# Optimization experiments

Hardware: AMD Instinct MI355X
Metric: run time of the kernel (lower is better)

The kernel has to match this reference:

```python
import jax, jax.numpy as jnp
import numpy as np

N_EMBD = 1024
N_HEAD = 16
HEAD_DIM = N_EMBD // N_HEAD


def setup_inputs() -> dict:
    key = jax.random.key(0)
    ks = jax.random.split(key, 5)
    B, T, C = 2, 2048, N_EMBD
    scale = 0.02
    return {
        "x": jax.random.normal(ks[0], (B, T, C), dtype=jnp.float32),
        "w_attn": jax.random.normal(ks[1], (C, 3 * C), dtype=jnp.float32) * scale,
        "b_attn": jax.random.normal(ks[2], (3 * C,), dtype=jnp.float32) * scale,
        "w_proj": jax.random.normal(ks[3], (C, C), dtype=jnp.float32) * scale,
        "b_proj": jax.random.normal(ks[4], (C,), dtype=jnp.float32) * scale,
    }


def reference(x, w_attn, b_attn, w_proj, b_proj):
    B, T, C = x.shape
    H, D = N_HEAD, HEAD_DIM
    qkv = x @ w_attn + b_attn  # [B,T,3C]
    q, k, v = jnp.split(qkv, 3, axis=-1)
    # [B,T,C] -> [B,H,T,D]
    q = q.reshape(B, T, H, D).transpose(0, 2, 1, 3)
    k = k.reshape(B, T, H, D).transpose(0, 2, 1, 3)
    v = v.reshape(B, T, H, D).transpose(0, 2, 1, 3)
    scores = jnp.einsum("bhqd,bhkd->bhqk", q, k) / jnp.sqrt(jnp.float32(D))
    causal = jnp.tril(jnp.ones((T, T), dtype=bool))
    scores = jnp.where(causal, scores, jnp.finfo(scores.dtype).min)
    attn = jax.nn.softmax(scores, axis=-1)
    y = jnp.einsum("bhqk,bhkd->bhqd", attn, v)  # [B,H,T,D]
    y = y.transpose(0, 2, 1, 3).reshape(B, T, C)
    return y @ w_proj + b_proj
```

## Files before the change

### kernel.cpp

```cpp
#include <hip/hip_runtime.h>

typedef unsigned short u16;
typedef u16 u16x4 __attribute__((ext_vector_type(4)));
typedef u16 u16x8 __attribute__((ext_vector_type(8)));
typedef __bf16 bf16x8 __attribute__((ext_vector_type(8)));
typedef float floatx4 __attribute__((ext_vector_type(4)));

#define N_EMBD 1024
#define N_HEAD 16
#define HEAD_DIM 64
#define SEQ 2048
#define BATCH 2
#define M_ROWS (BATCH * SEQ)

typedef __attribute__((address_space(1))) const unsigned char ga_t;
typedef __attribute__((address_space(3))) unsigned char la_t;

#if __has_builtin(__builtin_amdgcn_exp2f)
#define EXP2(x) __builtin_amdgcn_exp2f(x)
#else
#define EXP2(x) exp2f(x)
#endif

__device__ __forceinline__ float bf2f(u16 b) {
  return __uint_as_float(((unsigned)b) << 16);
}
__device__ __forceinline__ u16 f2bf(float f) {
  unsigned u = __float_as_uint(f);
  u += 0x7fffu + ((u >> 16) & 1u);
  return (u16)(u >> 16);
}

__global__ __launch_bounds__(256) void convert_x(const float* __restrict__ x,
                                                 u16* __restrict__ xb) {
  const long i = ((long)blockIdx.x * 256 + threadIdx.x) * 8;
  const float4 f0 = *(const float4*)&x[i];
  const float4 f1 = *(const float4*)&x[i + 4];
  u16x8 p;
  p[0] = f2bf(f0.x); p[1] = f2bf(f0.y); p[2] = f2bf(f0.z); p[3] = f2bf(f0.w);
  p[4] = f2bf(f1.x); p[5] = f2bf(f1.y); p[6] = f2bf(f1.z); p[7] = f2bf(f1.w);
  *(u16x8*)&xb[i] = p;
}

__global__ __launch_bounds__(256) void transpose2(
    const float* __restrict__ wa, const float* __restrict__ wp,
    u16* __restrict__ outa, u16* __restrict__ outp) {
  __shared__ u16 tile[32][33];
  const int R = N_EMBD;
  const float* in;
  u16* out;
  int C, bx;
  if (blockIdx.x < 96) {
    in = wa; out = outa; C = 3 * N_EMBD; bx = blockIdx.x * 32;
  } else {
    in = wp; out = outp; C = N_EMBD; bx = (blockIdx.x - 96) * 32;
  }
  const int by = blockIdx.y * 32;
  const int tx = threadIdx.x;
  const int ty = threadIdx.y;
#pragma unroll
  for (int j = 0; j < 32; j += 8)
    tile[ty + j][tx] = f2bf(in[(long)(by + ty + j) * C + bx + tx]);
  __syncthreads();
#pragma unroll
  for (int j = 0; j < 32; j += 8)
    out[(long)(bx + ty + j) * R + by + tx] = tile[tx][ty + j];
}

#define BK 32

template <int MODE>
__global__ __launch_bounds__(256) void gemm128(
    const u16* __restrict__ A, const u16* __restrict__ Bt,
    const float* __restrict__ bias, float* __restrict__ out,
    u16* __restrict__ qo, u16* __restrict__ ko, u16* __restrict__ vo, int N,
    int K) {
  __shared__ u16 As[128 * BK];
  __shared__ u16 Bs[128 * BK];
  const int tid = threadIdx.x;
  const int bm = blockIdx.y * 128;
  const int bn = blockIdx.x * 128;
  const int w = tid >> 6;
  const int l = tid & 63;
  const int wm = (w >> 1) * 64;
  const int wn = (w & 1) * 64;
  const int m16 = l & 15;
  const int quad = l >> 4;
  const int lrow = l >> 2;
  const int lcol = (l & 3) * 8;

  floatx4 acc[4][4];
#pragma unroll
  for (int i = 0; i < 4; ++i)
#pragma unroll
    for (int j = 0; j < 4; ++j) acc[i][j] = (floatx4){0.f, 0.f, 0.f, 0.f};

  for (int kt = 0; kt < K; kt += BK) {
#pragma unroll
    for (int p = 0; p < 2; ++p) {
      const int arow = p * 64 + w * 16;
      long gA;
      if (MODE == 0) {
        gA = (long)(bm + arow + lrow) * K + kt + lcol;
      } else {
        const int m = bm + arow + lrow;
        const int b = m >> 11, t = m & 2047;
        const int k0 = kt + lcol;
        const int head = k0 >> 6, dd = k0 & 63;
        gA = (((long)(b * N_HEAD + head)) * SEQ + t) * HEAD_DIM + dd;
      }
      __builtin_amdgcn_global_load_lds((ga_t*)(A + gA), (la_t*)&As[arow * BK],
                                       16, 0, 0);
      const long gB = (long)(bn + arow + lrow) * K + kt + lcol;
      __builtin_amdgcn_global_load_lds((ga_t*)(Bt + gB), (la_t*)&Bs[arow * BK],
                                       16, 0, 0);
    }
    __syncthreads();

    bf16x8 af[4], bfr[4];
#pragma unroll
    for (int i = 0; i < 4; ++i)
      af[i] = __builtin_bit_cast(
          bf16x8, *(const u16x8*)&As[(wm + i * 16 + m16) * BK + quad * 8]);
#pragma unroll
    for (int j = 0; j < 4; ++j)
      bfr[j] = __builtin_bit_cast(
          bf16x8, *(const u16x8*)&Bs[(wn + j * 16 + m16) * BK + quad * 8]);
#pragma unroll
    for (int i = 0; i < 4; ++i)
#pragma unroll
      for (int j = 0; j < 4; ++j)
        acc[i][j] = __builtin_amdgcn_mfma_f32_16x16x32_bf16(af[i], bfr[j],
                                                            acc[i][j], 0, 0, 0);
    __syncthreads();
  }

#pragma unroll
  for (int i = 0; i < 4; ++i) {
#pragma unroll
    for (int j = 0; j < 4; ++j) {
      const int col = bn + wn + j * 16 + m16;
      const float bv = bias[col];
      if (MODE == 1) {
#pragma unroll
        for (int r = 0; r < 4; ++r) {
          const int row = bm + wm + i * 16 + quad * 4 + r;
          out[(long)row * N_EMBD + col] = acc[i][j][r] + bv;
        }
      } else {
        const int which = col >> 10;
        const int cc = col & 1023;
        const int h = cc >> 6;
        const int dd = cc & 63;
        const int row0 = bm + wm + i * 16 + quad * 4;
        const int b = row0 >> 11;
        const int t0 = row0 & 2047;
        if (which == 2) {
          u16x4 pk;
#pragma unroll
          for (int r = 0; r < 4; ++r) pk[r] = f2bf(acc[i][j][r] + bv);
          *(u16x4*)&vo[(((long)(b * N_HEAD + h)) * HEAD_DIM + dd) * SEQ + t0] =
              pk;
        } else {
          u16* dst = (which == 0) ? qo : ko;
#pragma unroll
          for (int r = 0; r < 4; ++r)
            dst[(((long)(b * N_HEAD + h)) * SEQ + t0 + r) * HEAD_DIM + dd] =
                f2bf(acc[i][j][r] + bv);
        }
      }
    }
  }
}

#define BQ 64
#define BKV 64
#define KPAD 72
#define LOG2E 1.44269504f
#define NQT (SEQ / BQ)

__device__ __forceinline__ void load_kv(const u16* __restrict__ K,
                                        const u16* __restrict__ Vt, long bh,
                                        int kt, int tid, u16x8 kreg[2],
                                        u16x8 vreg[2]) {
#pragma unroll
  for (int i = 0; i < 2; ++i) {
    const int p = tid + 256 * i;
    const int kkey = p >> 3, kdg = p & 7;
    kreg[i] = *(const u16x8*)&K[(bh * SEQ + kt + kkey) * HEAD_DIM + kdg * 8];
    const int vd = p >> 3, vkg = (p & 7) * 8;
    vreg[i] = *(const u16x8*)&Vt[(bh * HEAD_DIM + vd) * SEQ + kt + vkg];
  }
}

__global__ __launch_bounds__(256) void flash_attn(u16* __restrict__ Qy,
                                                  const u16* __restrict__ K,
                                                  const u16* __restrict__ Vt) {
  const int pidx = blockIdx.x;
  const int h = blockIdx.y;
  const int b = blockIdx.z;
  const long bh = b * N_HEAD + h;
  const int tid = threadIdx.x;
  const int w = tid >> 6;
  const int l = tid & 63;
  const int m16 = l & 15;
  const int quad = l >> 4;

  __shared__ u16 Kl[2][BKV * KPAD];
  __shared__ u16 Vl[2][HEAD_DIM * KPAD];
  __shared__ u16 Pl[4][16 * KPAD];

  const float SC = 0.125f * LOG2E;

  for (int ph = 0; ph < 2; ++ph) {
    const int iq = (ph == 0) ? pidx : (NQT - 1 - pidx);
    const int qb = iq * BQ;
    const int ntiles = iq + 1;
    const int qglob = qb + w * 16 + m16;

    bf16x8 qf[2];
    {
      const u16* qrow = Qy + (bh * SEQ + qglob) * HEAD_DIM;
      qf[0] = __builtin_bit_cast(bf16x8, *(const u16x8*)&qrow[quad * 8]);
      qf[1] = __builtin_bit_cast(bf16x8, *(const u16x8*)&qrow[32 + quad * 8]);
    }

    floatx4 Oacc[4];
#pragma unroll
    for (int t = 0; t < 4; ++t) Oacc[t] = (floatx4){0.f, 0.f, 0.f, 0.f};
    float mrow = -1e30f, lrow = 0.f;

    u16x8 kreg[2], vreg[2];
    load_kv(K, Vt, bh, 0, tid, kreg, vreg);

    for (int it = 0; it < ntiles; ++it) {
      const int buf = it & 1;
#pragma unroll
      for (int i = 0; i < 2; ++i) {
        const int p = tid + 256 * i;
        const int kkey = p >> 3, kdg = p & 7;
        *(u16x8*)&Kl[buf][kkey * KPAD + kdg * 8] = kreg[i];
        const int vd = p >> 3, vkg = (p & 7) * 8;
        *(u16x8*)&Vl[buf][vd * KPAD + vkg] = vreg[i];
      }
      __syncthreads();
      if (it + 1 < ntiles) load_kv(K, Vt, bh, (it + 1) * BKV, tid, kreg, vreg);

      floatx4 s[4];
#pragma unroll
      for (int j = 0; j < 4; ++j) s[j] = (floatx4){0.f, 0.f, 0.f, 0.f};
#pragma unroll
      for (int j = 0; j < 4; ++j)
#pragma unroll
        for (int kk = 0; kk < 2; ++kk) {
          const bf16x8 kf = __builtin_bit_cast(
              bf16x8, *(const u16x8*)&Kl[buf][(j * 16 + m16) * KPAD + kk * 32 +
                                              quad * 8]);
          s[j] = __builtin_amdgcn_mfma_f32_16x16x32_bf16(kf, qf[kk], s[j], 0,
                                                         0, 0);
        }
      if (it == ntiles - 1) {
        const int kt = it * BKV;
#pragma unroll
        for (int j = 0; j < 4; ++j) {
          const int key0 = kt + j * 16 + quad * 4;
#pragma unroll
          for (int r = 0; r < 4; ++r)
            if (key0 + r > qglob) s[j][r] = -1e30f;
        }
      }

      float tm = s[0][0];
#pragma unroll
      for (int j = 0; j < 4; ++j)
#pragma unroll
        for (int r = 0; r < 4; ++r) tm = fmaxf(tm, s[j][r]);
      tm = fmaxf(tm, __shfl_xor(tm, 16, 64));
      tm = fmaxf(tm, __shfl_xor(tm, 32, 64));
      const float mn = fmaxf(mrow, tm * SC);
      const float al = EXP2(mrow - mn);
      mrow = mn;

      float ls = 0.f;
#pragma unroll
      for (int j = 0; j < 4; ++j) {
        u16x4 pk;
#pragma unroll
        for (int r = 0; r < 4; ++r) {
          const float p = EXP2(__builtin_fmaf(s[j][r], SC, -mn));
          ls += p;
          pk[r] = f2bf(p);
        }
        *(u16x4*)&Pl[w][m16 * KPAD + j * 16 + quad * 4] = pk;
      }
      ls += __shfl_xor(ls, 16, 64);
      ls += __shfl_xor(ls, 32, 64);
      lrow = lrow * al + ls;
#pragma unroll
      for (int t = 0; t < 4; ++t)
#pragma unroll
        for (int r = 0; r < 4; ++r) Oacc[t][r] *= al;

      bf16x8 pf[2];
      pf[0] = __builtin_bit_cast(bf16x8,
                                 *(const u16x8*)&Pl[w][m16 * KPAD + quad * 8]);
      pf[1] = __builtin_bit_cast(
          bf16x8, *(const u16x8*)&Pl[w][m16 * KPAD + 32 + quad * 8]);
#pragma unroll
      for (int t = 0; t < 4; ++t)
#pragma unroll
        for (int kk = 0; kk < 2; ++kk) {
          const bf16x8 vf = __builtin_bit_cast(
              bf16x8, *(const u16x8*)&Vl[buf][(t * 16 + m16) * KPAD + kk * 32 +
                                              quad * 8]);
          Oacc[t] = __builtin_amdgcn_mfma_f32_16x16x32_bf16(vf, pf[kk],
                                                            Oacc[t], 0, 0, 0);
        }
    }

    const float invl = 1.f / lrow;
#pragma unroll
    for (int t = 0; t < 4; ++t) {
      u16x4 pk;
#pragma unroll
      for (int r = 0; r < 4; ++r) pk[r] = f2bf(Oacc[t][r] * invl);
      *(u16x4*)&Qy[(bh * SEQ + qglob) * HEAD_DIM + t * 16 + quad * 4] = pk;
    }
    __syncthreads();
  }
}

extern "C" void kernel_launch(void* const* d_in, const int* in_sizes, int n_in,
                              void* d_out, int out_size, void* d_ws,
                              size_t ws_size, hipStream_t stream) {
  const float* x = (const float*)d_in[0];
  const float* w_attn = (const float*)d_in[1];
  const float* b_attn = (const float*)d_in[2];
  const float* w_proj = (const float*)d_in[3];
  const float* b_proj = (const float*)d_in[4];
  float* out = (float*)d_out;

  char* ws = (char*)d_ws;
  const size_t SZ = (size_t)BATCH * N_HEAD * SEQ * HEAD_DIM * sizeof(u16);
  u16* q = (u16*)(ws);
  u16* k = (u16*)(ws + SZ);
  u16* vT = (u16*)(ws + 2 * SZ);
  u16* wT_a = (u16*)(ws + 3 * SZ);
  u16* wT_p = (u16*)(ws + 3 * SZ + (size_t)3 * N_EMBD * N_EMBD * sizeof(u16));
  u16* xb = (u16*)(ws + 3 * SZ + (size_t)4 * N_EMBD * N_EMBD * sizeof(u16));

  convert_x<<<(long)M_ROWS * N_EMBD / 8 / 256, 256, 0, stream>>>(x, xb);
  transpose2<<<dim3(128, 32), dim3(32, 8), 0, stream>>>(w_attn, w_proj, wT_a,
                                                        wT_p);

  gemm128<0><<<dim3(3 * N_EMBD / 128, M_ROWS / 128), 256, 0, stream>>>(
      xb, wT_a, b_attn, nullptr, q, k, vT, 3 * N_EMBD, N_EMBD);

  flash_attn<<<dim3(NQT / 2, N_HEAD, BATCH), 256, 0, stream>>>(q, k, vT);

  gemm128<1><<<dim3(N_EMBD / 128, M_ROWS / 128), 256, 0, stream>>>(
      q, wT_p, b_proj, out, nullptr, nullptr, nullptr, N_EMBD, N_EMBD);
}
```

Baseline: 197.3 us.

## Merge prep kernels, use hardware bf16 convert, reschedule flash attention longest-first

```diff
diff --git a/kernel.cpp b/kernel.cpp
--- a/kernel.cpp
+++ b/kernel.cpp
@@ -22,45 +22,48 @@
 #define EXP2(x) exp2f(x)
 #endif
 
-__device__ __forceinline__ float bf2f(u16 b) {
-  return __uint_as_float(((unsigned)b) << 16);
-}
-__device__ __forceinline__ u16 f2bf(float f) {
-  unsigned u = __float_as_uint(f);
-  u += 0x7fffu + ((u >> 16) & 1u);
-  return (u16)(u >> 16);
-}
-
-__global__ __launch_bounds__(256) void convert_x(const float* __restrict__ x,
-                                                 u16* __restrict__ xb) {
-  const long i = ((long)blockIdx.x * 256 + threadIdx.x) * 8;
-  const float4 f0 = *(const float4*)&x[i];
-  const float4 f1 = *(const float4*)&x[i + 4];
-  u16x8 p;
-  p[0] = f2bf(f0.x); p[1] = f2bf(f0.y); p[2] = f2bf(f0.z); p[3] = f2bf(f0.w);
-  p[4] = f2bf(f1.x); p[5] = f2bf(f1.y); p[6] = f2bf(f1.z); p[7] = f2bf(f1.w);
-  *(u16x8*)&xb[i] = p;
-}
-
-__global__ __launch_bounds__(256) void transpose2(
-    const float* __restrict__ wa, const float* __restrict__ wp,
-    u16* __restrict__ outa, u16* __restrict__ outp) {
+__device__ __forceinline__ u16 cvt_bf16(float f) {
+  return __builtin_bit_cast(u16, (__bf16)f);
+}
+
+__global__ __launch_bounds__(256) void prep(const float* __restrict__ x,
+                                            u16* __restrict__ xb,
+                                            const float* __restrict__ wa,
+                                            const float* __restrict__ wp,
+                                            u16* __restrict__ outa,
+                                            u16* __restrict__ outp) {
+  const int bid = blockIdx.x;
+  if (bid < 2048) {
+    const long i = ((long)bid * 256 + threadIdx.x) * 8;
+    const float4 f0 = *(const float4*)&x[i];
+    const float4 f1 = *(const float4*)&x[i + 4];
+    u16x8 p;
+    p[0] = cvt_bf16(f0.x); p[1] = cvt_bf16(f0.y);
+    p[2] = cvt_bf16(f0.z); p[3] = cvt_bf16(f0.w);
+    p[4] = cvt_bf16(f1.x); p[5] = cvt_bf16(f1.y);
+    p[6] = cvt_bf16(f1.z); p[7] = cvt_bf16(f1.w);
+    *(u16x8*)&xb[i] = p;
+    return;
+  }
   __shared__ u16 tile[32][33];
+  const int t = bid - 2048;
+  const int gx = t & 127;
+  const int gy = t >> 7;
   const int R = N_EMBD;
   const float* in;
   u16* out;
   int C, bx;
-  if (blockIdx.x < 96) {
-    in = wa; out = outa; C = 3 * N_EMBD; bx = blockIdx.x * 32;
+  if (gx < 96) {
+    in = wa; out = outa; C = 3 * N_EMBD; bx = gx * 32;
   } else {
-    in = wp; out = outp; C = N_EMBD; bx = (blockIdx.x - 96) * 32;
-  }
-  const int by = blockIdx.y * 32;
-  const int tx = threadIdx.x;
-  const int ty = threadIdx.y;
+    in = wp; out = outp; C = N_EMBD; bx = (gx - 96) * 32;
+  }
+  const int by = gy * 32;
+  const int tx = threadIdx.x & 31;
+  const int ty = threadIdx.x >> 5;
 #pragma unroll
   for (int j = 0; j < 32; j += 8)
-    tile[ty + j][tx] = f2bf(in[(long)(by + ty + j) * C + bx + tx]);
+    tile[ty + j][tx] = cvt_bf16(in[(long)(by + ty + j) * C + bx + tx]);
   __syncthreads();
 #pragma unroll
   for (int j = 0; j < 32; j += 8)
@@ -158,7 +161,7 @@
         if (which == 2) {
           u16x4 pk;
 #pragma unroll
-          for (int r = 0; r < 4; ++r) pk[r] = f2bf(acc[i][j][r] + bv);
+          for (int r = 0; r < 4; ++r) pk[r] = cvt_bf16(acc[i][j][r] + bv);
           *(u16x4*)&vo[(((long)(b * N_HEAD + h)) * HEAD_DIM + dd) * SEQ + t0] =
               pk;
         } else {
@@ -166,7 +169,7 @@
 #pragma unroll
           for (int r = 0; r < 4; ++r)
             dst[(((long)(b * N_HEAD + h)) * SEQ + t0 + r) * HEAD_DIM + dd] =
-                f2bf(acc[i][j][r] + bv);
+                cvt_bf16(acc[i][j][r] + bv);
         }
       }
     }
@@ -196,10 +199,10 @@
 __global__ __launch_bounds__(256) void flash_attn(u16* __restrict__ Qy,
                                                   const u16* __restrict__ K,
                                                   const u16* __restrict__ Vt) {
-  const int pidx = blockIdx.x;
-  const int h = blockIdx.y;
-  const int b = blockIdx.z;
-  const long bh = b * N_HEAD + h;
+  const int id = blockIdx.x;
+  const int iq = (NQT - 1) - (id >> 5);
+  const int bh_ = ((id >> 3) & 3) * 8 + (id & 7);
+  const long bh = bh_;
   const int tid = threadIdx.x;
   const int w = tid >> 6;
   const int l = tid & 63;
@@ -212,121 +215,117 @@
 
   const float SC = 0.125f * LOG2E;
 
-  for (int ph = 0; ph < 2; ++ph) {
-    const int iq = (ph == 0) ? pidx : (NQT - 1 - pidx);
-    const int qb = iq * BQ;
-    const int ntiles = iq + 1;
-    const int qglob = qb + w * 16 + m16;
-
-    bf16x8 qf[2];
-    {
-      const u16* qrow = Qy + (bh * SEQ + qglob) * HEAD_DIM;
-      qf[0] = __builtin_bit_cast(bf16x8, *(const u16x8*)&qrow[quad * 8]);
-      qf[1] = __builtin_bit_cast(bf16x8, *(const u16x8*)&qrow[32 + quad * 8]);
-    }
-
-    floatx4 Oacc[4];
-#pragma unroll
-    for (int t = 0; t < 4; ++t) Oacc[t] = (floatx4){0.f, 0.f, 0.f, 0.f};
-    float mrow = -1e30f, lrow = 0.f;
-
-    u16x8 kreg[2], vreg[2];
-    load_kv(K, Vt, bh, 0, tid, kreg, vreg);
-
-    for (int it = 0; it < ntiles; ++it) {
-      const int buf = it & 1;
-#pragma unroll
-      for (int i = 0; i < 2; ++i) {
-        const int p = tid + 256 * i;
-        const int kkey = p >> 3, kdg = p & 7;
-        *(u16x8*)&Kl[buf][kkey * KPAD + kdg * 8] = kreg[i];
-        const int vd = p >> 3, vkg = (p & 7) * 8;
-        *(u16x8*)&Vl[buf][vd * KPAD + vkg] = vreg[i];
-      }
-      __syncthreads();
-      if (it + 1 < ntiles) load_kv(K, Vt, bh, (it + 1) * BKV, tid, kreg, vreg);
-
-      floatx4 s[4];
-#pragma unroll
-      for (int j = 0; j < 4; ++j) s[j] = (floatx4){0.f, 0.f, 0.f, 0.f};
-#pragma unroll
-      for (int j = 0; j < 4; ++j)
-#pragma unroll
-        for (int kk = 0; kk < 2; ++kk) {
-          const bf16x8 kf = __builtin_bit_cast(
-              bf16x8, *(const u16x8*)&Kl[buf][(j * 16 + m16) * KPAD + kk * 32 +
-                                              quad * 8]);
-          s[j] = __builtin_amdgcn_mfma_f32_16x16x32_bf16(kf, qf[kk], s[j], 0,
-                                                         0, 0);
-        }
-      if (it == ntiles - 1) {
-        const int kt = it * BKV;
-#pragma unroll
-        for (int j = 0; j < 4; ++j) {
-          const int key0 = kt + j * 16 + quad * 4;
-#pragma unroll
-          for (int r = 0; r < 4; ++r)
-            if (key0 + r > qglob) s[j][r] = -1e30f;
-        }
-      }
-
-      float tm = s[0][0];
-#pragma unroll
-      for (int j = 0; j < 4; ++j)
-#pragma unroll
-        for (int r = 0; r < 4; ++r) tm = fmaxf(tm, s[j][r]);
-      tm = fmaxf(tm, __shfl_xor(tm, 16, 64));
-      tm = fmaxf(tm, __shfl_xor(tm, 32, 64));
-      const float mn = fmaxf(mrow, tm * SC);
-      const float al = EXP2(mrow - mn);
-      mrow = mn;
-
-      float ls = 0.f;
+  const int qb = iq * BQ;
+  const int ntiles = iq + 1;
+  const int qglob = qb + w * 16 + m16;
+
+  bf16x8 qf[2];
+  {
+    const u16* qrow = Qy + (bh * SEQ + qglob) * HEAD_DIM;
+    qf[0] = __builtin_bit_cast(bf16x8, *(const u16x8*)&qrow[quad * 8]);
+    qf[1] = __builtin_bit_cast(bf16x8, *(const u16x8*)&qrow[32 + quad * 8]);
+  }
+
+  floatx4 Oacc[4];
+#pragma unroll
+  for (int t = 0; t < 4; ++t) Oacc[t] = (floatx4){0.f, 0.f, 0.f, 0.f};
+  float mrow = -1e30f, lrow = 0.f;
+
+  u16x8 kreg[2], vreg[2];
+  load_kv(K, Vt, bh, 0, tid, kreg, vreg);
+
+  for (int it = 0; it < ntiles; ++it) {
+    const int buf = it & 1;
+#pragma unroll
+    for (int i = 0; i < 2; ++i) {
+      const int p = tid + 256 * i;
+      const int kkey = p >> 3, kdg = p & 7;
+      *(u16x8*)&Kl[buf][kkey * KPAD + kdg * 8] = kreg[i];
+      const int vd = p >> 3, vkg = (p & 7) * 8;
+      *(u16x8*)&Vl[buf][vd * KPAD + vkg] = vreg[i];
+    }
+    __syncthreads();
+    if (it + 1 < ntiles) load_kv(K, Vt, bh, (it + 1) * BKV, tid, kreg, vreg);
+
+    floatx4 s[4];
+#pragma unroll
+    for (int j = 0; j < 4; ++j) s[j] = (floatx4){0.f, 0.f, 0.f, 0.f};
+#pragma unroll
+    for (int j = 0; j < 4; ++j)
+#pragma unroll
+      for (int kk = 0; kk < 2; ++kk) {
+        const bf16x8 kf = __builtin_bit_cast(
+            bf16x8, *(const u16x8*)&Kl[buf][(j * 16 + m16) * KPAD + kk * 32 +
+                                            quad * 8]);
+        s[j] = __builtin_amdgcn_mfma_f32_16x16x32_bf16(kf, qf[kk], s[j], 0, 0,
+                                                       0);
+      }
+    if (it == ntiles - 1) {
+      const int kt = it * BKV;
 #pragma unroll
       for (int j = 0; j < 4; ++j) {
-        u16x4 pk;
-#pragma unroll
-        for (int r = 0; r < 4; ++r) {
-          const float p = EXP2(__builtin_fmaf(s[j][r], SC, -mn));
-          ls += p;
-          pk[r] = f2bf(p);
-        }
-        *(u16x4*)&Pl[w][m16 * KPAD + j * 16 + quad * 4] = pk;
-      }
-      ls += __shfl_xor(ls, 16, 64);
-      ls += __shfl_xor(ls, 32, 64);
-      lrow = lrow * al + ls;
-#pragma unroll
-      for (int t = 0; t < 4; ++t)
-#pragma unroll
-        for (int r = 0; r < 4; ++r) Oacc[t][r] *= al;
-
-      bf16x8 pf[2];
-      pf[0] = __builtin_bit_cast(bf16x8,
-                                 *(const u16x8*)&Pl[w][m16 * KPAD + quad * 8]);
-      pf[1] = __builtin_bit_cast(
-          bf16x8, *(const u16x8*)&Pl[w][m16 * KPAD + 32 + quad * 8]);
-#pragma unroll
-      for (int t = 0; t < 4; ++t)
-#pragma unroll
-        for (int kk = 0; kk < 2; ++kk) {
-          const bf16x8 vf = __builtin_bit_cast(
-              bf16x8, *(const u16x8*)&Vl[buf][(t * 16 + m16) * KPAD + kk * 32 +
-                                              quad * 8]);
-          Oacc[t] = __builtin_amdgcn_mfma_f32_16x16x32_bf16(vf, pf[kk],
-                                                            Oacc[t], 0, 0, 0);
-        }
-    }
-
-    const float invl = 1.f / lrow;
-#pragma unroll
-    for (int t = 0; t < 4; ++t) {
+        const int key0 = kt + j * 16 + quad * 4;
+#pragma unroll
+        for (int r = 0; r < 4; ++r)
+          if (key0 + r > qglob) s[j][r] = -1e30f;
+      }
+    }
+
+    float tm = s[0][0];
+#pragma unroll
+    for (int j = 0; j < 4; ++j)
+#pragma unroll
+      for (int r = 0; r < 4; ++r) tm = fmaxf(tm, s[j][r]);
+    tm = fmaxf(tm, __shfl_xor(tm, 16, 64));
+    tm = fmaxf(tm, __shfl_xor(tm, 32, 64));
+    const float mn = fmaxf(mrow, tm * SC);
+    const float al = EXP2(mrow - mn);
+    mrow = mn;
+
+    float ls = 0.f;
+#pragma unroll
+    for (int j = 0; j < 4; ++j) {
       u16x4 pk;
 #pragma unroll
-      for (int r = 0; r < 4; ++r) pk[r] = f2bf(Oacc[t][r] * invl);
-      *(u16x4*)&Qy[(bh * SEQ + qglob) * HEAD_DIM + t * 16 + quad * 4] = pk;
-    }
-    __syncthreads();
+      for (int r = 0; r < 4; ++r) {
+        const float p = EXP2(__builtin_fmaf(s[j][r], SC, -mn));
+        ls += p;
+        pk[r] = cvt_bf16(p);
+      }
+      *(u16x4*)&Pl[w][m16 * KPAD + j * 16 + quad * 4] = pk;
+    }
+    ls += __shfl_xor(ls, 16, 64);
+    ls += __shfl_xor(ls, 32, 64);
+    lrow = lrow * al + ls;
+#pragma unroll
+    for (int t = 0; t < 4; ++t)
+#pragma unroll
+      for (int r = 0; r < 4; ++r) Oacc[t][r] *= al;
+
+    bf16x8 pf[2];
+    pf[0] = __builtin_bit_cast(bf16x8,
+                               *(const u16x8*)&Pl[w][m16 * KPAD + quad * 8]);
+    pf[1] = __builtin_bit_cast(
+        bf16x8, *(const u16x8*)&Pl[w][m16 * KPAD + 32 + quad * 8]);
+#pragma unroll
+    for (int t = 0; t < 4; ++t)
+#pragma unroll
+      for (int kk = 0; kk < 2; ++kk) {
+        const bf16x8 vf = __builtin_bit_cast(
+            bf16x8, *(const u16x8*)&Vl[buf][(t * 16 + m16) * KPAD + kk * 32 +
+                                            quad * 8]);
+        Oacc[t] = __builtin_amdgcn_mfma_f32_16x16x32_bf16(vf, pf[kk], Oacc[t],
+                                                          0, 0, 0);
+      }
+  }
+
+  const float invl = 1.f / lrow;
+#pragma unroll
+  for (int t = 0; t < 4; ++t) {
+    u16x4 pk;
+#pragma unroll
+    for (int r = 0; r < 4; ++r) pk[r] = cvt_bf16(Oacc[t][r] * invl);
+    *(u16x4*)&Qy[(bh * SEQ + qglob) * HEAD_DIM + t * 16 + quad * 4] = pk;
   }
 }
 
@@ -349,14 +348,12 @@
   u16* wT_p = (u16*)(ws + 3 * SZ + (size_t)3 * N_EMBD * N_EMBD * sizeof(u16));
   u16* xb = (u16*)(ws + 3 * SZ + (size_t)4 * N_EMBD * N_EMBD * sizeof(u16));
 
-  convert_x<<<(long)M_ROWS * N_EMBD / 8 / 256, 256, 0, stream>>>(x, xb);
-  transpose2<<<dim3(128, 32), dim3(32, 8), 0, stream>>>(w_attn, w_proj, wT_a,
-                                                        wT_p);
+  prep<<<2048 + 4096, 256, 0, stream>>>(x, xb, w_attn, w_proj, wT_a, wT_p);
 
   gemm128<0><<<dim3(3 * N_EMBD / 128, M_ROWS / 128), 256, 0, stream>>>(
       xb, wT_a, b_attn, nullptr, q, k, vT, 3 * N_EMBD, N_EMBD);
 
-  flash_attn<<<dim3(NQT / 2, N_HEAD, BATCH), 256, 0, stream>>>(q, k, vT);
+  flash_attn<<<NQT * 32, 256, 0, stream>>>(q, k, vT);
 
   gemm128<1><<<dim3(N_EMBD / 128, M_ROWS / 128), 256, 0, stream>>>(
       q, wT_p, b_proj, out, nullptr, nullptr, nullptr, N_EMBD, N_EMBD);
```

Result: faster. 188.4 us (-4.5%).
